# Optimization experiments

Hardware: AMD Instinct MI355X
Metric: run time of the kernel (lower is better)

Reference implementation:

```python
import jax, jax.numpy as jnp
import numpy as np


def setup_inputs() -> dict:
    key = jax.random.key(0)
    k1, k2, k3, k4, k5 = jax.random.split(key, 5)
    B, S, D_IN, D_OUT = 4, 2048, 4096, 4096
    inp = jax.random.normal(k1, (B, S, D_IN), dtype=jnp.float32)
    w_q = jax.random.randint(k2, (D_OUT, D_IN), 0, 255, dtype=jnp.int32)
    scale = jax.random.uniform(k3, (D_OUT, 1), dtype=jnp.float32) * 0.02 + 1e-3
    zero_point = jax.random.randint(k4, (D_OUT, 1), 0, 255, dtype=jnp.int32)
    bias = jax.random.normal(k5, (D_OUT,), dtype=jnp.float32)
    return {"input": inp, "w_q": w_q, "scale": scale, "zero_point": zero_point, "bias": bias}


def reference(input, w_q, scale, zero_point, bias):
    # decompress_module: dequantize int weight with per-output-channel affine params
    # W[o, i] = (w_q[o, i] - zp[o]) * scale[o]   -> full fp32 weight materialized
    W = (w_q - zero_point).astype(jnp.float32) * scale  # [D_OUT, D_IN]
    # F.linear: y = x @ W^T + b
    return jnp.einsum("bsi,oi->bso", input, W) + bias
```

## Files before the change

kernel.cpp:

```cpp
#include <hip/hip_runtime.h>
#include <hip/hip_bf16.h>
#include <stdint.h>

typedef float  f32x4  __attribute__((ext_vector_type(4)));
typedef float  f32x16 __attribute__((ext_vector_type(16)));
typedef unsigned int   u32x4 __attribute__((ext_vector_type(4)));
typedef unsigned short u16x4 __attribute__((ext_vector_type(4)));
typedef int    i32x4  __attribute__((ext_vector_type(4)));

__device__ inline unsigned short f2bf(float f) {
  unsigned int u = __builtin_bit_cast(unsigned int, f);
  u += 0x7fffu + ((u >> 16) & 1u);
  return (unsigned short)(u >> 16);
}

__device__ inline void mfma32x32x16bf16(f32x16& acc, u32x4 a, u32x4 b) {
  asm volatile("v_mfma_f32_32x32x16_bf16 %0, %1, %2, %0"
               : "+v"(acc)
               : "v"(a), "v"(b));
}

__device__ inline void mfma16x16x32bf16(f32x4& acc, u32x4 a, u32x4 b) {
  asm volatile("v_mfma_f32_16x16x32_bf16 %0, %1, %2, %0"
               : "+v"(acc)
               : "v"(a), "v"(b));
}

__device__ inline void gload16(const unsigned short* src, char* ldsdst) {
  __builtin_amdgcn_global_load_lds(
      (const __attribute__((address_space(1))) void*)src,
      (__attribute__((address_space(3))) void*)ldsdst, 16, 0, 0);
}


__global__ __launch_bounds__(256) void prep_x(const float* __restrict__ x,
                                              unsigned short* __restrict__ xb,
                                              int K, int KT) {
  const int rb = blockIdx.x / KT;
  const int kt = blockIdx.x % KT;
  __shared__ unsigned short t[256 * 64];
  const int tid = threadIdx.x;
  const int klane = tid & 15;
  const int rbase = tid >> 4;
  const float* src = x + (size_t)(rb * 256) * K + kt * 64;
  const int gw = klane >> 1, hw = klane & 1;
  for (int it = 0; it < 16; ++it) {
    int row = it * 16 + rbase;
    f32x4 v = *(const f32x4*)(src + (size_t)row * K + klane * 4);
    u16x4 h;
    h[0] = f2bf(v[0]); h[1] = f2bf(v[1]); h[2] = f2bf(v[2]); h[3] = f2bf(v[3]);
    *(u16x4*)&t[row * 64 + ((gw ^ (row & 7)) << 3) + hw * 4] = h;
  }
  __syncthreads();
  unsigned short* dst = xb + ((size_t)rb * KT + kt) * 16384;
  for (int j = 0; j < 8; ++j) {
    int c = j * 256 + tid;
    int l = c & 63, f = (c >> 6) & 7, s = c >> 9;
    int row = f * 32 + (l & 31);
    int g   = (s * 2 + (l >> 5)) ^ (row & 7);
    u32x4 v = *(const u32x4*)&t[row * 64 + (g << 3)];
    *(u32x4*)(dst + (size_t)c * 8) = v;
  }
}

__global__ __launch_bounds__(256) void prep_w(const int* __restrict__ wq,
                                              const int* __restrict__ zp,
                                              unsigned short* __restrict__ wb,
                                              int K, int KT) {
  const int cb = blockIdx.x / KT;
  const int kt = blockIdx.x % KT;
  __shared__ unsigned short t[256 * 64];
  const int tid = threadIdx.x;
  const int klane = tid & 15;
  const int rbase = tid >> 4;
  const int* src = wq + (size_t)(cb * 256) * K + kt * 64;
  const int gw = klane >> 1, hw = klane & 1;
  for (int it = 0; it < 16; ++it) {
    int row = it * 16 + rbase;
    i32x4 v = *(const i32x4*)(src + (size_t)row * K + klane * 4);
    int z = zp[cb * 256 + row];
    u16x4 h;
    h[0] = f2bf((float)(v[0] - z)); h[1] = f2bf((float)(v[1] - z));
    h[2] = f2bf((float)(v[2] - z)); h[3] = f2bf((float)(v[3] - z));
    *(u16x4*)&t[row * 64 + ((gw ^ (row & 7)) << 3) + hw * 4] = h;
  }
  __syncthreads();
  unsigned short* dst = wb + ((size_t)cb * KT + kt) * 16384;
  for (int j = 0; j < 8; ++j) {
    int c = j * 256 + tid;
    int l = c & 63, f = (c >> 6) & 7, s = c >> 9;
    int row = f * 32 + (l & 31);
    int g   = (s * 2 + (l >> 5)) ^ (row & 7);
    u32x4 v = *(const u32x4*)&t[row * 64 + (g << 3)];
    *(u32x4*)(dst + (size_t)c * 8) = v;
  }
}

__global__ __launch_bounds__(512, 2) void gemm_ring(
    const unsigned short* __restrict__ xb, const unsigned short* __restrict__ wb,
    const float* __restrict__ scale, const float* __restrict__ bias,
    float* __restrict__ out, int N, int KT) {

  __shared__ unsigned short lds[65536];

  const int NB = N >> 8;
  const int nwg = gridDim.x;
  const int wg  = (blockIdx.x & 7) * (nwg >> 3) + (blockIdx.x >> 3);
  const int rb = wg / NB;
  const int cb = wg % NB;

  const int tid  = threadIdx.x;
  const int lane = tid & 63;
  const int wave = tid >> 6;
  const int wr = wave >> 2;
  const int wc = wave & 3;
  const int wr4 = wr * 4, wc2 = wc * 2;
  const int lane16 = lane * 16;

  const unsigned short* xtb = xb + (size_t)rb * (KT >> 1) * 16384;
  const unsigned short* wtb = wb + (size_t)cb * (KT >> 1) * 16384;

  f32x16 acc[4][2] = {};

  auto STAGE = [&](int u) {
    const int slot = (u & 3) << 15;
    const unsigned short* as = xtb + (size_t)u * 8192;
    const unsigned short* bs = wtb + (size_t)u * 8192;
    char* da = (char*)lds + slot + wave * 2048;
    char* db = (char*)lds + slot + 16384 + wave * 2048;
    gload16(as + wave * 1024 + lane * 8, da);
    gload16(as + wave * 1024 + 512 + lane * 8, da + 1024);
    gload16(bs + wave * 1024 + lane * 8, db);
    gload16(bs + wave * 1024 + 512 + lane * 8, db + 1024);
  };

  auto LDA = [&](int slotb, int s, int m) -> u32x4 {
    return *(const u32x4*)((const char*)lds + slotb + s * 8192 +
                           (wr4 + m) * 1024 + lane16);
  };
  auto LDB = [&](int slotb, int s, int n) -> u32x4 {
    return *(const u32x4*)((const char*)lds + slotb + 16384 + s * 8192 +
                           (wc2 + n) * 1024 + lane16);
  };

#define BODY(U, VM, ST)                                                        \
  {                                                                            \
    const int u_ = (U);                                                        \
    const int sb = (u_ & 3) << 15;                                             \
    asm volatile("s_waitcnt vmcnt(" #VM ")" ::: "memory");                     \
    __builtin_amdgcn_s_barrier();                                              \
    if (ST) STAGE(u_ + 3);                                                     \
    u32x4 bfr[2][2];                                                           \
    _Pragma("unroll")                                                          \
    for (int s = 0; s < 2; ++s)                                                \
      _Pragma("unroll")                                                        \
      for (int n = 0; n < 2; ++n) bfr[s][n] = LDB(sb, s, n);                   \
    __builtin_amdgcn_s_setprio(1);                                             \
    _Pragma("unroll")                                                          \
    for (int s = 0; s < 2; ++s)                                                \
      _Pragma("unroll")                                                        \
      for (int m = 0; m < 4; ++m) {                                            \
        u32x4 a = LDA(sb, s, m);                                               \
        mfma32x32x16bf16(acc[m][0], a, bfr[s][0]);                             \
        mfma32x32x16bf16(acc[m][1], a, bfr[s][1]);                             \
      }                                                                        \
    __builtin_amdgcn_s_setprio(0);                                             \
  }

  STAGE(0); STAGE(1); STAGE(2);

  int u = 0;
  for (; u + 3 < KT; ++u) BODY(u, 8, true);
  BODY(u, 8, false); ++u;
  BODY(u, 4, false); ++u;
  BODY(u, 0, false);
#undef BODY

  const int m0 = rb * 256 + wr * 128;
  const int n0 = cb * 256 + wc * 64;
  const int l31 = lane & 31, lhi = lane >> 5;
#pragma unroll
  for (int n = 0; n < 2; ++n) {
    const int col = n0 + n * 32 + l31;
    const float sc = scale[col];
    const float bi = bias[col];
#pragma unroll
    for (int m = 0; m < 4; ++m) {
      f32x16 v = acc[m][n];
      const int rowb = m0 + m * 32 + 4 * lhi;
#pragma unroll
      for (int q = 0; q < 4; ++q)
#pragma unroll
        for (int r = 0; r < 4; ++r)
          out[(size_t)(rowb + q * 8 + r) * N + col] = v[q * 4 + r] * sc + bi;
    }
  }
}

__global__ __launch_bounds__(256) void gemm_fallback(
    const float* __restrict__ x, const int* __restrict__ wq, const int* __restrict__ zp,
    const float* __restrict__ scale, const float* __restrict__ bias,
    float* __restrict__ out, int M, int N, int K) {

  __shared__ unsigned short Alds[128 * 32];
  __shared__ unsigned short Blds[128 * 32];

  const int tid = threadIdx.x;
  const int ntile = N / 128;
  const int m0 = (blockIdx.x / ntile) * 128, n0 = (blockIdx.x % ntile) * 128;
  const int lane = tid & 63;
  const int wave = tid >> 6;
  const int wr = wave >> 1, wc = wave & 1;
  const int lr = lane & 15, lhi = lane >> 4;
  f32x4 acc[4][4] = {};
  const int ar = tid >> 3, ac4 = tid & 7;

  for (int k0 = 0; k0 < K; k0 += 32) {
#pragma unroll
    for (int p = 0; p < 4; ++p) {
      int r = p * 32 + ar;
      i32x4 w = *(const i32x4*)(wq + (size_t)(n0 + r) * K + k0 + ac4 * 4);
      int z = zp[n0 + r];
      u16x4 h;
      h[0] = f2bf((float)(w[0] - z)); h[1] = f2bf((float)(w[1] - z));
      h[2] = f2bf((float)(w[2] - z)); h[3] = f2bf((float)(w[3] - z));
      *(u16x4*)&Blds[r * 32 + ac4 * 4] = h;
    }
#pragma unroll
    for (int p = 0; p < 4; ++p) {
      int r = p * 32 + ar;
      f32x4 v = *(const f32x4*)(x + (size_t)(m0 + r) * K + k0 + ac4 * 4);
      u16x4 h;
      h[0] = f2bf(v[0]); h[1] = f2bf(v[1]); h[2] = f2bf(v[2]); h[3] = f2bf(v[3]);
      *(u16x4*)&Alds[r * 32 + ac4 * 4] = h;
    }
    __syncthreads();
    u32x4 af[4], bf[4];
#pragma unroll
    for (int i = 0; i < 4; ++i) {
      af[i] = *(const u32x4*)&Alds[(wr * 64 + i * 16 + lr) * 32 + lhi * 8];
      bf[i] = *(const u32x4*)&Blds[(wc * 64 + i * 16 + lr) * 32 + lhi * 8];
    }
#pragma unroll
    for (int i = 0; i < 4; ++i)
#pragma unroll
      for (int j = 0; j < 4; ++j)
        mfma16x16x32bf16(acc[i][j], af[i], bf[j]);
    __syncthreads();
  }
  const int crow0 = m0 + wr * 64;
  const int ccol0 = n0 + wc * 64 + lr;
#pragma unroll
  for (int j = 0; j < 4; ++j) {
    int col = ccol0 + j * 16;
    float sc = scale[col], bi = bias[col];
#pragma unroll
    for (int i = 0; i < 4; ++i) {
      int row = crow0 + i * 16 + lhi * 4;
      f32x4 v = acc[i][j];
#pragma unroll
      for (int r = 0; r < 4; ++r)
        out[(size_t)(row + r) * N + col] = v[r] * sc + bi;
    }
  }
}

extern "C" void kernel_launch(void* const* d_in, const int* in_sizes, int n_in,
                              void* d_out, int out_size, void* d_ws, size_t ws_size,
                              hipStream_t stream) {
  const float* x     = (const float*)d_in[0];
  const int*   wq    = (const int*)d_in[1];
  const float* scale = (const float*)d_in[2];
  const int*   zp    = (const int*)d_in[3];
  const float* bias  = (const float*)d_in[4];
  float* out = (float*)d_out;

  const int DOUT = in_sizes[4];
  const int DIN  = in_sizes[1] / DOUT;
  const int M    = in_sizes[0] / DIN;

  const size_t needX = (size_t)M * DIN * 2;
  const size_t needW = (size_t)DOUT * DIN * 2;

  const int nwg  = (M / 256) * (DOUT / 256);
  const int KT64 = DIN / 64;
  const int KT32 = DIN / 32;
  const bool shapes_ok = (M % 256 == 0) && (DOUT % 256 == 0) && (DIN % 64 == 0) &&
                         (nwg % 8 == 0) && (KT32 >= 8);

  if (shapes_ok && ws_size >= needX + needW) {
    unsigned short* xb = (unsigned short*)d_ws;
    unsigned short* wb = (unsigned short*)((char*)d_ws + needX);
    prep_x<<<(M / 256) * KT64, 256, 0, stream>>>(x, xb, DIN, KT64);
    prep_w<<<(DOUT / 256) * KT64, 256, 0, stream>>>(wq, zp, wb, DIN, KT64);
    gemm_ring<<<nwg, 512, 0, stream>>>(xb, wb, scale, bias, out, DOUT, KT32);
  } else {
    dim3 grid((M / 128) * (DOUT / 128));
    gemm_fallback<<<grid, 256, 0, stream>>>(x, wq, zp, scale, bias, out, M, DOUT, DIN);
  }
}
```

Measured before the change: 297.2 us.

## Load weight tiles directly into registers with double buffering, halving LDS

The weight (B) operand is no longer staged through shared memory. Each wave loads its B fragments straight from global memory into a pair of register buffers that ping-pong across iterations, while only the activation (A) tile still goes through the 4-slot LDS ring. This halves the LDS footprint, which may let more workgroups fit per CU, and removes the LDS write and read for B. In exchange, waves that share B columns fetch the same data from global/L2 twice. The barrier now comes before the vmcnt wait, which weakens the guarantee that other waves' LDS stages are visible. The loop is unrolled by two, so the host now requires an even K-tile count.

Measured after the change: 326.1 us. +9.7%, slower.

```diff
diff --git a/kernel.cpp b/kernel.cpp
--- a/kernel.cpp
+++ b/kernel.cpp
@@ -101,7 +101,7 @@
     const float* __restrict__ scale, const float* __restrict__ bias,
     float* __restrict__ out, int N, int KT) {
 
-  __shared__ unsigned short lds[65536];
+  __shared__ unsigned short lds[32768];
 
   const int NB = N >> 8;
   const int nwg = gridDim.x;
@@ -121,59 +121,67 @@
   const unsigned short* wtb = wb + (size_t)cb * (KT >> 1) * 16384;
 
   f32x16 acc[4][2] = {};
+  u32x4 bA[2][2], bB[2][2];
 
   auto STAGE = [&](int u) {
-    const int slot = (u & 3) << 15;
+    const int slot = (u & 3) << 14;
     const unsigned short* as = xtb + (size_t)u * 8192;
-    const unsigned short* bs = wtb + (size_t)u * 8192;
     char* da = (char*)lds + slot + wave * 2048;
-    char* db = (char*)lds + slot + 16384 + wave * 2048;
     gload16(as + wave * 1024 + lane * 8, da);
     gload16(as + wave * 1024 + 512 + lane * 8, da + 1024);
-    gload16(bs + wave * 1024 + lane * 8, db);
-    gload16(bs + wave * 1024 + 512 + lane * 8, db + 1024);
   };
 
   auto LDA = [&](int slotb, int s, int m) -> u32x4 {
     return *(const u32x4*)((const char*)lds + slotb + s * 8192 +
                            (wr4 + m) * 1024 + lane16);
   };
-  auto LDB = [&](int slotb, int s, int n) -> u32x4 {
-    return *(const u32x4*)((const char*)lds + slotb + 16384 + s * 8192 +
-                           (wc2 + n) * 1024 + lane16);
-  };
-
-#define BODY(U, VM, ST)                                                        \
+
+#define BODY(U, CUR, NXT, VM, DOB, DOS)                                        \
   {                                                                            \
     const int u_ = (U);                                                        \
-    const int sb = (u_ & 3) << 15;                                             \
+    const int sb = (u_ & 3) << 14;                                             \
+    __builtin_amdgcn_s_barrier();      \
+    if (DOB) {                                                                 \
+      const unsigned short* bsrc = wtb + (size_t)(u_ + 1) * 8192 + lane * 8;   \
+      _Pragma("unroll")                                                        \
+      for (int s = 0; s < 2; ++s)                                              \
+        _Pragma("unroll")                                                      \
+        for (int n = 0; n < 2; ++n)                                            \
+          NXT[s][n] = *(const u32x4*)(bsrc + s * 4096 + (wc2 + n) * 512);      \
+    }                                                                          \
+    if (DOS) STAGE(u_ + 3);                                                    \
     asm volatile("s_waitcnt vmcnt(" #VM ")" ::: "memory");                     \
-    __builtin_amdgcn_s_barrier();                                              \
-    if (ST) STAGE(u_ + 3);                                                     \
-    u32x4 bfr[2][2];                                                           \
-    _Pragma("unroll")                                                          \
-    for (int s = 0; s < 2; ++s)                                                \
-      _Pragma("unroll")                                                        \
-      for (int n = 0; n < 2; ++n) bfr[s][n] = LDB(sb, s, n);                   \
     __builtin_amdgcn_s_setprio(1);                                             \
     _Pragma("unroll")                                                          \
     for (int s = 0; s < 2; ++s)                                                \
       _Pragma("unroll")                                                        \
       for (int m = 0; m < 4; ++m) {                                            \
         u32x4 a = LDA(sb, s, m);                                               \
-        mfma32x32x16bf16(acc[m][0], a, bfr[s][0]);                             \
-        mfma32x32x16bf16(acc[m][1], a, bfr[s][1]);                             \
+        mfma32x32x16bf16(acc[m][0], a, CUR[s][0]);                             \
+        mfma32x32x16bf16(acc[m][1], a, CUR[s][1]);                             \
       }                                                                        \
     __builtin_amdgcn_s_setprio(0);                                             \
   }
 
+  {
+    const unsigned short* bsrc = wtb + lane * 8;
+#pragma unroll
+    for (int s = 0; s < 2; ++s)
+#pragma unroll
+      for (int n = 0; n < 2; ++n)
+        bA[s][n] = *(const u32x4*)(bsrc + s * 4096 + (wc2 + n) * 512);
+  }
   STAGE(0); STAGE(1); STAGE(2);
 
   int u = 0;
-  for (; u + 3 < KT; ++u) BODY(u, 8, true);
-  BODY(u, 8, false); ++u;
-  BODY(u, 4, false); ++u;
-  BODY(u, 0, false);
+  for (; u + 4 < KT; u += 2) {
+    BODY(u,     bA, bB, 8, true, true);
+    BODY(u + 1, bB, bA, 8, true, true);
+  }
+  BODY(u, bA, bB, 8, true,  true);  ++u;
+  BODY(u, bB, bA, 6, true,  false); ++u;
+  BODY(u, bA, bB, 4, true,  false); ++u;
+  BODY(u, bB, bA, 0, false, false);
 #undef BODY
 
   const int m0 = rb * 256 + wr * 128;
@@ -286,7 +294,7 @@
   const int KT64 = DIN / 64;
   const int KT32 = DIN / 32;
   const bool shapes_ok = (M % 256 == 0) && (DOUT % 256 == 0) && (DIN % 64 == 0) &&
-                         (nwg % 8 == 0) && (KT32 >= 8);
+                         (nwg % 8 == 0) && (KT32 >= 8) && (KT32 % 2 == 0);
 
   if (shapes_ok && ws_size >= needX + needW) {
     unsigned short* xb = (unsigned short*)d_ws;
```

## Process two K-stages per barrier with double-pair prefetch in ring GEMM

Applied to the files above, without the earlier changes.

Restructures the 4-slot LDS ring main loop so each barrier covers two K sub-tiles and issues two stage loads at once, halving the number of block barriers and waitcnt points. B fragments are now loaded per s-step right before use instead of all upfront, which lowers register pressure. The tradeoff is that the loop waits on vmcnt(0) every iteration, so prefetch depth drops from three stages in flight to about two. A K-tile-count parity check is added to the host shape guard.

New measurement: 297.9 us. No clear change (+0.3%).

```diff
diff --git a/kernel.cpp b/kernel.cpp
--- a/kernel.cpp
+++ b/kernel.cpp
@@ -143,38 +143,42 @@
                            (wc2 + n) * 1024 + lane16);
   };
 
-#define BODY(U, VM, ST)                                                        \
+#define SUBTILE(SB)                                                            \
   {                                                                            \
-    const int u_ = (U);                                                        \
-    const int sb = (u_ & 3) << 15;                                             \
-    asm volatile("s_waitcnt vmcnt(" #VM ")" ::: "memory");                     \
-    __builtin_amdgcn_s_barrier();                                              \
-    if (ST) STAGE(u_ + 3);                                                     \
-    u32x4 bfr[2][2];                                                           \
-    _Pragma("unroll")                                                          \
-    for (int s = 0; s < 2; ++s)                                                \
-      _Pragma("unroll")                                                        \
-      for (int n = 0; n < 2; ++n) bfr[s][n] = LDB(sb, s, n);                   \
+    const int sb_ = (SB);                                                      \
     __builtin_amdgcn_s_setprio(1);                                             \
     _Pragma("unroll")                                                          \
-    for (int s = 0; s < 2; ++s)                                                \
+    for (int s = 0; s < 2; ++s) {                                              \
+      u32x4 b0 = LDB(sb_, s, 0), b1 = LDB(sb_, s, 1);                          \
       _Pragma("unroll")                                                        \
       for (int m = 0; m < 4; ++m) {                                            \
-        u32x4 a = LDA(sb, s, m);                                               \
-        mfma32x32x16bf16(acc[m][0], a, bfr[s][0]);                             \
-        mfma32x32x16bf16(acc[m][1], a, bfr[s][1]);                             \
+        u32x4 a = LDA(sb_, s, m);                                              \
+        mfma32x32x16bf16(acc[m][0], a, b0);                                    \
+        mfma32x32x16bf16(acc[m][1], a, b1);                                    \
       }                                                                        \
+    }                                                                          \
     __builtin_amdgcn_s_setprio(0);                                             \
   }
 
-  STAGE(0); STAGE(1); STAGE(2);
-
-  int u = 0;
-  for (; u + 3 < KT; ++u) BODY(u, 8, true);
-  BODY(u, 8, false); ++u;
-  BODY(u, 4, false); ++u;
-  BODY(u, 0, false);
+#define BODY(V, ST)                                                            \
+  {                                                                            \
+    const int v_ = (V);                                                        \
+    const int u0 = v_ * 2, u1 = v_ * 2 + 1;                                    \
+    asm volatile("s_waitcnt vmcnt(0)" ::: "memory");                           \
+    __builtin_amdgcn_s_barrier();                                              \
+    if (ST) { STAGE(u0 + 2); STAGE(u0 + 3); }                                  \
+    SUBTILE((u0 & 3) << 15);                                                   \
+    SUBTILE((u1 & 3) << 15);                                                   \
+  }
+
+  STAGE(0); STAGE(1);
+
+  const int NBODY = KT >> 1;
+  int v = 0;
+  for (; v + 1 < NBODY; ++v) BODY(v, true);
+  BODY(v, false);
 #undef BODY
+#undef SUBTILE
 
   const int m0 = rb * 256 + wr * 128;
   const int n0 = cb * 256 + wc * 64;
@@ -186,13 +190,13 @@
     const float bi = bias[col];
 #pragma unroll
     for (int m = 0; m < 4; ++m) {
-      f32x16 v = acc[m][n];
+      f32x16 v2 = acc[m][n];
       const int rowb = m0 + m * 32 + 4 * lhi;
 #pragma unroll
       for (int q = 0; q < 4; ++q)
 #pragma unroll
         for (int r = 0; r < 4; ++r)
-          out[(size_t)(rowb + q * 8 + r) * N + col] = v[q * 4 + r] * sc + bi;
+          out[(size_t)(rowb + q * 8 + r) * N + col] = v2[q * 4 + r] * sc + bi;
     }
   }
 }
@@ -286,7 +290,7 @@
   const int KT64 = DIN / 64;
   const int KT32 = DIN / 32;
   const bool shapes_ok = (M % 256 == 0) && (DOUT % 256 == 0) && (DIN % 64 == 0) &&
-                         (nwg % 8 == 0) && (KT32 >= 8);
+                         (nwg % 8 == 0) && (KT32 >= 8) && (KT32 % 2 == 0);
 
   if (shapes_ok && ws_size >= needX + needW) {
     unsigned short* xb = (unsigned short*)d_ws;
```

## Split each K-step into two phases interleaving A/B prefetch with MFMA

Applied to the files above, without the earlier changes.

Restructures the main GEMM loop so each K-tile is processed in two half-phases (s=0,1). Each phase loads its A/B fragments from LDS up front, issues half of the next tile's global-to-LDS prefetch (A or B), then runs the eight MFMAs. The global-load wait moves to the end of the second phase. The intent is to spread memory issue more evenly across the MFMA work and overlap LDS reads with it. In exchange there are twice as many barriers per K-step and an explicit lgkmcnt(0) wait before each MFMA block.

Measured after the change: 299.1 us. About the same (+0.7%).

```diff
diff --git a/kernel.cpp b/kernel.cpp
--- a/kernel.cpp
+++ b/kernel.cpp
@@ -122,14 +122,17 @@
 
   f32x16 acc[4][2] = {};
 
-  auto STAGE = [&](int u) {
+  auto STAGE_A = [&](int u) {
     const int slot = (u & 3) << 15;
     const unsigned short* as = xtb + (size_t)u * 8192;
-    const unsigned short* bs = wtb + (size_t)u * 8192;
     char* da = (char*)lds + slot + wave * 2048;
-    char* db = (char*)lds + slot + 16384 + wave * 2048;
     gload16(as + wave * 1024 + lane * 8, da);
     gload16(as + wave * 1024 + 512 + lane * 8, da + 1024);
+  };
+  auto STAGE_B = [&](int u) {
+    const int slot = (u & 3) << 15;
+    const unsigned short* bs = wtb + (size_t)u * 8192;
+    char* db = (char*)lds + slot + 16384 + wave * 2048;
     gload16(bs + wave * 1024 + lane * 8, db);
     gload16(bs + wave * 1024 + 512 + lane * 8, db + 1024);
   };
@@ -143,38 +146,50 @@
                            (wc2 + n) * 1024 + lane16);
   };
 
-#define BODY(U, VM, ST)                                                        \
+#define PHASE(U, S, DRIP, VMASM)                                               \
   {                                                                            \
-    const int u_ = (U);                                                        \
-    const int sb = (u_ & 3) << 15;                                             \
-    asm volatile("s_waitcnt vmcnt(" #VM ")" ::: "memory");                     \
+    const int sb = ((U) & 3) << 15;                                            \
+    u32x4 b0 = LDB(sb, S, 0), b1 = LDB(sb, S, 1);                              \
+    u32x4 a0 = LDA(sb, S, 0), a1 = LDA(sb, S, 1);                              \
+    u32x4 a2 = LDA(sb, S, 2), a3 = LDA(sb, S, 3);                              \
+    DRIP;                                                                      \
     __builtin_amdgcn_s_barrier();                                              \
-    if (ST) STAGE(u_ + 3);                                                     \
-    u32x4 bfr[2][2];                                                           \
-    _Pragma("unroll")                                                          \
-    for (int s = 0; s < 2; ++s)                                                \
-      _Pragma("unroll")                                                        \
-      for (int n = 0; n < 2; ++n) bfr[s][n] = LDB(sb, s, n);                   \
+    asm volatile("s_waitcnt lgkmcnt(0)" ::: "memory");                         \
+    __builtin_amdgcn_sched_barrier(0);                                         \
     __builtin_amdgcn_s_setprio(1);                                             \
-    _Pragma("unroll")                                                          \
-    for (int s = 0; s < 2; ++s)                                                \
-      _Pragma("unroll")                                                        \
-      for (int m = 0; m < 4; ++m) {                                            \
-        u32x4 a = LDA(sb, s, m);                                               \
-        mfma32x32x16bf16(acc[m][0], a, bfr[s][0]);                             \
-        mfma32x32x16bf16(acc[m][1], a, bfr[s][1]);                             \
-      }                                                                        \
+    mfma32x32x16bf16(acc[0][0], a0, b0);                                       \
+    mfma32x32x16bf16(acc[0][1], a0, b1);                                       \
+    mfma32x32x16bf16(acc[1][0], a1, b0);                                       \
+    mfma32x32x16bf16(acc[1][1], a1, b1);                                       \
+    mfma32x32x16bf16(acc[2][0], a2, b0);                                       \
+    mfma32x32x16bf16(acc[2][1], a2, b1);                                       \
+    mfma32x32x16bf16(acc[3][0], a3, b0);                                       \
+    mfma32x32x16bf16(acc[3][1], a3, b1);                                       \
     __builtin_amdgcn_s_setprio(0);                                             \
-  }
-
-  STAGE(0); STAGE(1); STAGE(2);
+    VMASM;                                                                     \
+    __builtin_amdgcn_s_barrier();                                              \
+  }
+
+#define VM8 asm volatile("s_waitcnt vmcnt(8)" ::: "memory")
+#define VM4 asm volatile("s_waitcnt vmcnt(4)" ::: "memory")
+#define VM0 asm volatile("s_waitcnt vmcnt(0)" ::: "memory")
+
+  STAGE_A(0); STAGE_B(0); STAGE_A(1); STAGE_B(1); STAGE_A(2); STAGE_B(2);
+  asm volatile("s_waitcnt vmcnt(8)" ::: "memory");
+  __builtin_amdgcn_s_barrier();
 
   int u = 0;
-  for (; u + 3 < KT; ++u) BODY(u, 8, true);
-  BODY(u, 8, false); ++u;
-  BODY(u, 4, false); ++u;
-  BODY(u, 0, false);
-#undef BODY
+  for (; u + 3 < KT; ++u) {
+    PHASE(u, 0, STAGE_A(u + 3), );
+    PHASE(u, 1, STAGE_B(u + 3), VM8);
+  }
+  PHASE(u, 0, , );  PHASE(u, 1, , VM4); ++u;
+  PHASE(u, 0, , );  PHASE(u, 1, , VM0); ++u;
+  PHASE(u, 0, , );  PHASE(u, 1, , );
+#undef PHASE
+#undef VM8
+#undef VM4
+#undef VM0
 
   const int m0 = rb * 256 + wr * 128;
   const int n0 = cb * 256 + wc * 64;
```
